# Kernel optimization log

Measured on AMD Instinct MI355X. Metric: run time of the kernel, lower is better.

## Reference

```python
import jax, jax.numpy as jnp
import numpy as np

T, B, H, L = 256, 64, 1024, 2

def setup_inputs() -> dict:
    key = jax.random.key(0)
    ks = jax.random.split(key, 7)
    s = 1.0 / np.sqrt(H)  # torch LSTMCell init scale (uniform); randn*s keeps magnitudes sane
    return {
        "input_seq": jax.random.normal(ks[0], (T, B, H), jnp.float32),
        "h0": jax.random.normal(ks[1], (L, B, H), jnp.float32),
        "c0": jax.random.normal(ks[2], (L, B, H), jnp.float32),
        "W_ih": jax.random.normal(ks[3], (L, 4 * H, H), jnp.float32) * s,
        "W_hh": jax.random.normal(ks[4], (L, 4 * H, H), jnp.float32) * s,
        "b_ih": jax.random.normal(ks[5], (L, 4 * H), jnp.float32) * s,
        "b_hh": jax.random.normal(ks[6], (L, 4 * H), jnp.float32) * s,
    }

def _lstm_cell(x, h, c, w_ih, w_hh, bi, bh):
    # torch.nn.LSTMCell gate order: i, f, g, o
    gates = x @ w_ih.T + bi + h @ w_hh.T + bh  # [B, 4H]
    i, f, g, o = jnp.split(gates, 4, axis=-1)
    c_new = jax.nn.sigmoid(f) * c + jax.nn.sigmoid(i) * jnp.tanh(g)
    h_new = jax.nn.sigmoid(o) * jnp.tanh(c_new)
    return h_new, c_new

def reference(input_seq, h0, c0, W_ih, W_hh, b_ih, b_hh):
    def step(carry, x_t):
        h, c = carry  # each [L, B, H]
        new_h, new_c = [], []
        x = x_t
        for l in range(L):  # small fixed layer loop
            hl, cl = _lstm_cell(x, h[l], c[l], W_ih[l], W_hh[l], b_ih[l], b_hh[l])
            new_h.append(hl)
            new_c.append(cl)
            x = hl
        return (jnp.stack(new_h), jnp.stack(new_c)), None
    (h_fin, c_fin), _ = jax.lax.scan(step, (h0, c0), input_seq)
    return h_fin[-1]  # top-layer hidden at final timestep, [B, H]
```

## Files before the change

### kernel.cpp

```cpp
#include <hip/hip_runtime.h>

#define T_LEN 256
#define B_SZ  64
#define H_SZ  1024
#define G4H   4096
#define HB    (B_SZ * H_SZ)
#define NBLK  256
#define RING_SLOTS (T_LEN + 1)

typedef __attribute__((ext_vector_type(8))) short short8;
typedef __attribute__((ext_vector_type(4))) float float4_;
typedef __attribute__((ext_vector_type(4))) unsigned int uint4_;

__device__ __forceinline__ unsigned short bf16_rne(float x) {
  unsigned u = __builtin_bit_cast(unsigned, x);
  unsigned r = u + 0x7FFFu + ((u >> 16) & 1u);
  return (unsigned short)(r >> 16);
}
__device__ __forceinline__ float bf16_to_f32(unsigned short s) {
  unsigned u = ((unsigned)s) << 16;
  return __builtin_bit_cast(float, u);
}

__global__ __launch_bounds__(256)
void init_h(const float* __restrict__ h0, unsigned short* __restrict__ ringb,
            unsigned* __restrict__ bar) {
  if (blockIdx.x == 0) {
    #pragma unroll
    for (int j = 0; j < 4; ++j) bar[threadIdx.x * 4 + j] = 0u;
  }
  const int e0 = (blockIdx.x * 256 + threadIdx.x) * 4;
  #pragma unroll
  for (int j = 0; j < 4; ++j) {
    const int e = e0 + j;
    const int l = e >> 16;
    const int rem = e & (HB - 1);
    ringb[((size_t)l * RING_SLOTS + T_LEN) * HB + rem] = bf16_rne(h0[e]);
  }
}

__device__ __forceinline__ void wave_poll_chunk(const unsigned* slots16,
                                               unsigned v, int lane) {
  for (;;) {
    unsigned s = 0xFFFFFFFFu;
    if (lane < 16)
      s = __hip_atomic_load(slots16 + lane, __ATOMIC_RELAXED,
                            __HIP_MEMORY_SCOPE_AGENT);
    if (__all((int)(s >= v))) return;
    __builtin_amdgcn_s_sleep(1);
  }
}

__device__ __forceinline__ void mfma3(float4_ (&acc)[4][2],
                                      const short8& hi, const short8& lo,
                                      const short8 (&wp)[2][2][4],
                                      const int m, const int kb) {
  #pragma unroll
  for (int nt = 0; nt < 2; ++nt) {
    acc[m][nt] = __builtin_amdgcn_mfma_f32_16x16x32_bf16(hi, wp[0][nt][kb], acc[m][nt], 0, 0, 0);
    acc[m][nt] = __builtin_amdgcn_mfma_f32_16x16x32_bf16(lo, wp[0][nt][kb], acc[m][nt], 0, 0, 0);
    acc[m][nt] = __builtin_amdgcn_mfma_f32_16x16x32_bf16(hi, wp[1][nt][kb], acc[m][nt], 0, 0, 0);
  }
}

__device__ __forceinline__ void accum_hb(float4_ (&acc)[4][2],
                                         const unsigned short* src,
                                         const short8 (&wp)[2][2][4],
                                         const int nn, const int quad,
                                         const int wave) {
  const int kbase = wave * 128 + quad * 8;
  short8 va[8], vb[8];
  #pragma unroll
  for (int kb = 0; kb < 2; ++kb)
    #pragma unroll
    for (int m = 0; m < 4; ++m)
      va[kb * 4 + m] = *(const short8*)(src + (size_t)(m * 16 + nn) * H_SZ +
                                        kbase + kb * 32);
  #pragma unroll
  for (int kb = 0; kb < 2; ++kb)
    #pragma unroll
    for (int m = 0; m < 4; ++m)
      vb[kb * 4 + m] = *(const short8*)(src + (size_t)(m * 16 + nn) * H_SZ +
                                        kbase + (kb + 2) * 32);
  #pragma unroll
  for (int kb = 0; kb < 2; ++kb)
    #pragma unroll
    for (int m = 0; m < 4; ++m)
      #pragma unroll
      for (int nt = 0; nt < 2; ++nt) {
        acc[m][nt] = __builtin_amdgcn_mfma_f32_16x16x32_bf16(va[kb * 4 + m], wp[0][nt][kb], acc[m][nt], 0, 0, 0);
        acc[m][nt] = __builtin_amdgcn_mfma_f32_16x16x32_bf16(va[kb * 4 + m], wp[1][nt][kb], acc[m][nt], 0, 0, 0);
      }
  #pragma unroll
  for (int kb = 0; kb < 2; ++kb)
    #pragma unroll
    for (int m = 0; m < 4; ++m)
      #pragma unroll
      for (int nt = 0; nt < 2; ++nt) {
        acc[m][nt] = __builtin_amdgcn_mfma_f32_16x16x32_bf16(vb[kb * 4 + m], wp[0][nt][kb + 2], acc[m][nt], 0, 0, 0);
        acc[m][nt] = __builtin_amdgcn_mfma_f32_16x16x32_bf16(vb[kb * 4 + m], wp[1][nt][kb + 2], acc[m][nt], 0, 0, 0);
      }
}

__device__ __forceinline__ void accum_x(float4_ (&acc)[4][2],
                                        const float* src,
                                        const short8 (&wp)[2][2][4],
                                        const int nn, const int quad,
                                        const int wave) {
  #pragma unroll
  for (int kb = 0; kb < 4; ++kb) {
    const int k0 = wave * 128 + kb * 32 + quad * 8;
    #pragma unroll
    for (int m = 0; m < 4; ++m) {
      const float* p = src + (size_t)(m * 16 + nn) * H_SZ + k0;
      short8 hi, lo;
      #pragma unroll
      for (int j = 0; j < 8; ++j) {
        const float v = p[j];
        const unsigned short h = bf16_rne(v);
        hi[j] = (short)h;
        lo[j] = (short)bf16_rne(v - bf16_to_f32(h));
      }
      mfma3(acc, hi, lo, wp, m, kb);
    }
  }
}

__global__ __launch_bounds__(512, 1)
void lstm_persist(const float* __restrict__ x_in,
                  const float* __restrict__ c0_in,
                  const float* __restrict__ Wih,
                  const float* __restrict__ Whh,
                  const float* __restrict__ bih,
                  const float* __restrict__ bhh,
                  unsigned short* __restrict__ ringb,
                  float* __restrict__ out,
                  unsigned* __restrict__ bar)
{
  const int wg   = blockIdx.x;
  const int tid  = threadIdx.x;
  const int lane = tid & 63;
  const int wave = tid >> 6;

  const int layer = wg >> 7;
  const int cb    = wg & 127;
  const int nn    = lane & 15;
  const int quad  = lane >> 4;

  __shared__ float lds[8][64][36];

  int growA[2];
  #pragma unroll
  for (int nt = 0; nt < 2; ++nt) {
    const int q = nt * 2 + (nn >> 3);
    growA[nt] = q * H_SZ + cb * 8 + (nn & 7);
  }

  short8 wreg[2][2][2][4];
  #pragma unroll
  for (int mat = 0; mat < 2; ++mat) {
    const float* wsrc = mat ? Whh : Wih;
    #pragma unroll
    for (int nt = 0; nt < 2; ++nt)
      #pragma unroll
      for (int kb = 0; kb < 4; ++kb) {
        const float* p = wsrc + ((size_t)layer * G4H + growA[nt]) * H_SZ +
                         wave * 128 + kb * 32 + quad * 8;
        short8 hi, lo;
        #pragma unroll
        for (int j = 0; j < 8; ++j) {
          const float v = p[j];
          const unsigned short h = bf16_rne(v);
          hi[j] = (short)h;
          lo[j] = (short)bf16_rne(v - bf16_to_f32(h));
        }
        wreg[mat][0][nt][kb] = hi;
        wreg[mat][1][nt][kb] = lo;
      }
  }

  const int eb   = tid >> 2;
  const int ec   = (tid & 3) * 2;
  const int ecol = cb * 8 + ec;
  float4_ biasA, biasB;
  #pragma unroll
  for (int q = 0; q < 4; ++q) {
    biasA[q] = bih[layer * G4H + q * H_SZ + ecol] +
               bhh[layer * G4H + q * H_SZ + ecol];
    biasB[q] = bih[layer * G4H + q * H_SZ + ecol + 1] +
               bhh[layer * G4H + q * H_SZ + ecol + 1];
  }

  unsigned*       slotp     = bar + layer * 128 + cb;
  const unsigned* chunk_own = bar + layer * 128 + wave * 16;
  const unsigned* chunk_l0  = bar + wave * 16;

  const unsigned short* ring_own = ringb + (size_t)layer * RING_SLOTS * HB;
  const unsigned short* ring_l0  = ringb;

  float cA = 0.f, cB = 0.f;
  float4_ acc[4][2];
  #pragma unroll
  for (int m = 0; m < 4; ++m)
    #pragma unroll
    for (int nt = 0; nt < 2; ++nt)
      acc[m][nt] = float4_{0.f, 0.f, 0.f, 0.f};

  if (layer == 0) {
    accum_x(acc, x_in, wreg[0], nn, quad, wave);
  } else {
    wave_poll_chunk(chunk_l0, 1u, lane);
    accum_hb(acc, ring_l0 , wreg[0], nn, quad, wave);
  }

  #pragma unroll 1
  for (int t = 0; t < T_LEN; ++t) {
    if (t > 0)
      wave_poll_chunk(chunk_own, (unsigned)t, lane);

    accum_hb(acc, ring_own + (size_t)(t ? t - 1 : T_LEN) * HB,
             wreg[1], nn, quad, wave);

    #pragma unroll
    for (int m = 0; m < 4; ++m)
      #pragma unroll
      for (int nt = 0; nt < 2; ++nt)
        #pragma unroll
        for (int r = 0; r < 4; ++r)
          lds[wave][m * 16 + quad * 4 + r]
             [((nn & 7) << 2) + nt * 2 + (nn >> 3)] = acc[m][nt][r];
    __syncthreads();

    if (tid < 256) {
      float4_ gA = biasA, gB = biasB;
      #pragma unroll
      for (int w = 0; w < 8; ++w) {
        gA += *(const float4_*)&lds[w][eb][ec * 4];
        gB += *(const float4_*)&lds[w][eb][ec * 4 + 4];
      }
      float cpA, cpB;
      if (t == 0) {
        cpA = c0_in[(size_t)layer * HB + (size_t)eb * H_SZ + ecol];
        cpB = c0_in[(size_t)layer * HB + (size_t)eb * H_SZ + ecol + 1];
      } else { cpA = cA; cpB = cB; }
      const float igA = 1.f / (1.f + __expf(-gA[0]));
      const float fgA = 1.f / (1.f + __expf(-gA[1]));
      const float ggA = tanhf(gA[2]);
      const float ogA = 1.f / (1.f + __expf(-gA[3]));
      const float cnA = fgA * cpA + igA * ggA;
      const float hnA = ogA * tanhf(cnA);
      const float igB = 1.f / (1.f + __expf(-gB[0]));
      const float fgB = 1.f / (1.f + __expf(-gB[1]));
      const float ggB = tanhf(gB[2]);
      const float ogB = 1.f / (1.f + __expf(-gB[3]));
      const float cnB = fgB * cpB + igB * ggB;
      const float hnB = ogB * tanhf(cnB);
      cA = cnA; cB = cnB;
      const size_t ridx = ((size_t)layer * RING_SLOTS + t) * HB +
                          (size_t)eb * H_SZ + ecol;
      const unsigned pk = (unsigned)bf16_rne(hnA) |
                          ((unsigned)bf16_rne(hnB) << 16);
      __hip_atomic_store((unsigned*)(ringb + ridx), pk,
                         __ATOMIC_RELAXED, __HIP_MEMORY_SCOPE_AGENT);
      if (layer == 1 && t == T_LEN - 1) {
        out[(size_t)eb * H_SZ + ecol]     = hnA;
        out[(size_t)eb * H_SZ + ecol + 1] = hnB;
      }
    }

    __syncthreads();
    if (tid == 0) {
      __builtin_amdgcn_s_waitcnt(0);
      __hip_atomic_store(slotp, (unsigned)(t + 1),
                         __ATOMIC_RELAXED, __HIP_MEMORY_SCOPE_AGENT);
    }

    if (t < T_LEN - 1) {
      #pragma unroll
      for (int m = 0; m < 4; ++m)
        #pragma unroll
        for (int nt = 0; nt < 2; ++nt)
          acc[m][nt] = float4_{0.f, 0.f, 0.f, 0.f};
      if (layer == 0) {
        accum_x(acc, x_in + (size_t)(t + 1) * HB, wreg[0], nn, quad, wave);
      } else {
        wave_poll_chunk(chunk_l0, (unsigned)(t + 2), lane);
        accum_hb(acc, ring_l0 + (size_t)(t + 1) * HB,
                 wreg[0], nn, quad, wave);
      }
    }
  }
}

extern "C" void kernel_launch(void* const* d_in, const int* in_sizes, int n_in,
                              void* d_out, int out_size, void* d_ws, size_t ws_size,
                              hipStream_t stream) {
  (void)in_sizes; (void)n_in; (void)out_size; (void)ws_size;
  const float* x   = (const float*)d_in[0];
  const float* h0  = (const float*)d_in[1];
  const float* c0  = (const float*)d_in[2];
  const float* Wih = (const float*)d_in[3];
  const float* Whh = (const float*)d_in[4];
  const float* bih = (const float*)d_in[5];
  const float* bhh = (const float*)d_in[6];
  float* out = (float*)d_out;

  char* w = (char*)d_ws;
  unsigned short* ringb = (unsigned short*)w;
  unsigned*       bar   = (unsigned*)(w + (size_t)2 * RING_SLOTS * HB * 2);

  init_h<<<2 * HB / 4 / 256, 256, 0, stream>>>(h0, ringb, bar);
  lstm_persist<<<NBLK, 512, 0, stream>>>(x, c0, Wih, Whh, bih, bhh,
                                         ringb, out, bar);
}
```

Baseline: 4.284 ms.

## Use per-wave completion flags, double-buffer LDS, and pre-pack x into bf16 hi/lo

Each block previously published one step flag after a second __syncthreads. Now each of the four elementwise waves publishes its own sub-flag once its stores drain, and consumers poll 64 flags per wave. The gate LDS buffer is double-buffered by timestep parity so the trailing block barrier can be dropped. Separately, a new pre-kernel splits x into packed bf16 hi/lo pairs, so the recurrent loop only does a wide load and byte permutes instead of per-element conversion. The cost is an extra full pass over x, a larger workspace, and wider polling traffic.

After: 3.675 ms. 14.2% less time.

```diff
diff --git a/kernel.cpp b/kernel.cpp
--- a/kernel.cpp
+++ b/kernel.cpp
@@ -11,6 +11,7 @@
 typedef __attribute__((ext_vector_type(8))) short short8;
 typedef __attribute__((ext_vector_type(4))) float float4_;
 typedef __attribute__((ext_vector_type(4))) unsigned int uint4_;
+typedef __attribute__((ext_vector_type(8))) unsigned int uint8_;
 
 __device__ __forceinline__ unsigned short bf16_rne(float x) {
   unsigned u = __builtin_bit_cast(unsigned, x);
@@ -20,6 +21,20 @@
 __device__ __forceinline__ float bf16_to_f32(unsigned short s) {
   unsigned u = ((unsigned)s) << 16;
   return __builtin_bit_cast(float, u);
+}
+
+__global__ __launch_bounds__(256)
+void pack_x(const float* __restrict__ src, unsigned* __restrict__ dst) {
+  const size_t i = ((size_t)blockIdx.x * 256 + threadIdx.x) * 4;
+  float4_ v = *(const float4_*)(src + i);
+  uint4_ o;
+  #pragma unroll
+  for (int j = 0; j < 4; ++j) {
+    const unsigned short h = bf16_rne(v[j]);
+    const unsigned short l = bf16_rne(v[j] - bf16_to_f32(h));
+    o[j] = (unsigned)h | ((unsigned)l << 16);
+  }
+  *(uint4_*)(dst + i) = o;
 }
 
 __global__ __launch_bounds__(256)
@@ -39,27 +54,13 @@
   }
 }
 
-__device__ __forceinline__ void wave_poll_chunk(const unsigned* slots16,
-                                               unsigned v, int lane) {
+__device__ __forceinline__ void wave_poll64(const unsigned* s64, unsigned v,
+                                            int lane) {
   for (;;) {
-    unsigned s = 0xFFFFFFFFu;
-    if (lane < 16)
-      s = __hip_atomic_load(slots16 + lane, __ATOMIC_RELAXED,
-                            __HIP_MEMORY_SCOPE_AGENT);
+    const unsigned s = __hip_atomic_load(s64 + lane, __ATOMIC_RELAXED,
+                                         __HIP_MEMORY_SCOPE_AGENT);
     if (__all((int)(s >= v))) return;
     __builtin_amdgcn_s_sleep(1);
-  }
-}
-
-__device__ __forceinline__ void mfma3(float4_ (&acc)[4][2],
-                                      const short8& hi, const short8& lo,
-                                      const short8 (&wp)[2][2][4],
-                                      const int m, const int kb) {
-  #pragma unroll
-  for (int nt = 0; nt < 2; ++nt) {
-    acc[m][nt] = __builtin_amdgcn_mfma_f32_16x16x32_bf16(hi, wp[0][nt][kb], acc[m][nt], 0, 0, 0);
-    acc[m][nt] = __builtin_amdgcn_mfma_f32_16x16x32_bf16(lo, wp[0][nt][kb], acc[m][nt], 0, 0, 0);
-    acc[m][nt] = __builtin_amdgcn_mfma_f32_16x16x32_bf16(hi, wp[1][nt][kb], acc[m][nt], 0, 0, 0);
   }
 }
 
@@ -69,65 +70,55 @@
                                          const int nn, const int quad,
                                          const int wave) {
   const int kbase = wave * 128 + quad * 8;
-  short8 va[8], vb[8];
-  #pragma unroll
-  for (int kb = 0; kb < 2; ++kb)
+  short8 v[16];
+  #pragma unroll
+  for (int kb = 0; kb < 4; ++kb)
     #pragma unroll
     for (int m = 0; m < 4; ++m)
-      va[kb * 4 + m] = *(const short8*)(src + (size_t)(m * 16 + nn) * H_SZ +
-                                        kbase + kb * 32);
-  #pragma unroll
-  for (int kb = 0; kb < 2; ++kb)
+      v[kb * 4 + m] = *(const short8*)(src + (size_t)(m * 16 + nn) * H_SZ +
+                                       kbase + kb * 32);
+  #pragma unroll
+  for (int kb = 0; kb < 4; ++kb)
     #pragma unroll
     for (int m = 0; m < 4; ++m)
-      vb[kb * 4 + m] = *(const short8*)(src + (size_t)(m * 16 + nn) * H_SZ +
-                                        kbase + (kb + 2) * 32);
-  #pragma unroll
-  for (int kb = 0; kb < 2; ++kb)
-    #pragma unroll
-    for (int m = 0; m < 4; ++m)
       #pragma unroll
       for (int nt = 0; nt < 2; ++nt) {
-        acc[m][nt] = __builtin_amdgcn_mfma_f32_16x16x32_bf16(va[kb * 4 + m], wp[0][nt][kb], acc[m][nt], 0, 0, 0);
-        acc[m][nt] = __builtin_amdgcn_mfma_f32_16x16x32_bf16(va[kb * 4 + m], wp[1][nt][kb], acc[m][nt], 0, 0, 0);
-      }
-  #pragma unroll
-  for (int kb = 0; kb < 2; ++kb)
-    #pragma unroll
-    for (int m = 0; m < 4; ++m)
-      #pragma unroll
-      for (int nt = 0; nt < 2; ++nt) {
-        acc[m][nt] = __builtin_amdgcn_mfma_f32_16x16x32_bf16(vb[kb * 4 + m], wp[0][nt][kb + 2], acc[m][nt], 0, 0, 0);
-        acc[m][nt] = __builtin_amdgcn_mfma_f32_16x16x32_bf16(vb[kb * 4 + m], wp[1][nt][kb + 2], acc[m][nt], 0, 0, 0);
-      }
-}
-
-__device__ __forceinline__ void accum_x(float4_ (&acc)[4][2],
-                                        const float* src,
-                                        const short8 (&wp)[2][2][4],
-                                        const int nn, const int quad,
-                                        const int wave) {
+        acc[m][nt] = __builtin_amdgcn_mfma_f32_16x16x32_bf16(v[kb * 4 + m], wp[0][nt][kb], acc[m][nt], 0, 0, 0);
+        acc[m][nt] = __builtin_amdgcn_mfma_f32_16x16x32_bf16(v[kb * 4 + m], wp[1][nt][kb], acc[m][nt], 0, 0, 0);
+      }
+}
+
+__device__ __forceinline__ void accum_xp(float4_ (&acc)[4][2],
+                                         const unsigned* src,
+                                         const short8 (&wp)[2][2][4],
+                                         const int nn, const int quad,
+                                         const int wave) {
   #pragma unroll
   for (int kb = 0; kb < 4; ++kb) {
     const int k0 = wave * 128 + kb * 32 + quad * 8;
     #pragma unroll
     for (int m = 0; m < 4; ++m) {
-      const float* p = src + (size_t)(m * 16 + nn) * H_SZ + k0;
-      short8 hi, lo;
-      #pragma unroll
-      for (int j = 0; j < 8; ++j) {
-        const float v = p[j];
-        const unsigned short h = bf16_rne(v);
-        hi[j] = (short)h;
-        lo[j] = (short)bf16_rne(v - bf16_to_f32(h));
-      }
-      mfma3(acc, hi, lo, wp, m, kb);
+      const uint8_ u = *(const uint8_*)(src + (size_t)(m * 16 + nn) * H_SZ + k0);
+      uint4_ h4, l4;
+      #pragma unroll
+      for (int r = 0; r < 4; ++r) {
+        h4[r] = __builtin_amdgcn_perm(u[2 * r + 1], u[2 * r], 0x05040100u);
+        l4[r] = __builtin_amdgcn_perm(u[2 * r + 1], u[2 * r], 0x07060302u);
+      }
+      const short8 hi = __builtin_bit_cast(short8, h4);
+      const short8 lo = __builtin_bit_cast(short8, l4);
+      #pragma unroll
+      for (int nt = 0; nt < 2; ++nt) {
+        acc[m][nt] = __builtin_amdgcn_mfma_f32_16x16x32_bf16(hi, wp[0][nt][kb], acc[m][nt], 0, 0, 0);
+        acc[m][nt] = __builtin_amdgcn_mfma_f32_16x16x32_bf16(lo, wp[0][nt][kb], acc[m][nt], 0, 0, 0);
+        acc[m][nt] = __builtin_amdgcn_mfma_f32_16x16x32_bf16(hi, wp[1][nt][kb], acc[m][nt], 0, 0, 0);
+      }
     }
   }
 }
 
 __global__ __launch_bounds__(512, 1)
-void lstm_persist(const float* __restrict__ x_in,
+void lstm_persist(const unsigned* __restrict__ xp,
                   const float* __restrict__ c0_in,
                   const float* __restrict__ Wih,
                   const float* __restrict__ Whh,
@@ -147,7 +138,7 @@
   const int nn    = lane & 15;
   const int quad  = lane >> 4;
 
-  __shared__ float lds[8][64][36];
+  __shared__ float lds[2][8][64][36];
 
   int growA[2];
   #pragma unroll
@@ -179,8 +170,8 @@
       }
   }
 
-  const int eb   = tid >> 2;
-  const int ec   = (tid & 3) * 2;
+  const int eb   = wave * 16 + (lane >> 2);
+  const int ec   = (lane & 3) * 2;
   const int ecol = cb * 8 + ec;
   float4_ biasA, biasB;
   #pragma unroll
@@ -191,9 +182,9 @@
                bhh[layer * G4H + q * H_SZ + ecol + 1];
   }
 
-  unsigned*       slotp     = bar + layer * 128 + cb;
-  const unsigned* chunk_own = bar + layer * 128 + wave * 16;
-  const unsigned* chunk_l0  = bar + wave * 16;
+  unsigned*       subflag   = bar + layer * 512 + cb * 4 + wave;
+  const unsigned* chunk_own = bar + layer * 512 + wave * 64;
+  const unsigned* chunk_l0  = bar + wave * 64;
 
   const unsigned short* ring_own = ringb + (size_t)layer * RING_SLOTS * HB;
   const unsigned short* ring_l0  = ringb;
@@ -207,36 +198,37 @@
       acc[m][nt] = float4_{0.f, 0.f, 0.f, 0.f};
 
   if (layer == 0) {
-    accum_x(acc, x_in, wreg[0], nn, quad, wave);
+    accum_xp(acc, xp, wreg[0], nn, quad, wave);
   } else {
-    wave_poll_chunk(chunk_l0, 1u, lane);
+    wave_poll64(chunk_l0, 1u, lane);
     accum_hb(acc, ring_l0 , wreg[0], nn, quad, wave);
   }
 
   #pragma unroll 1
   for (int t = 0; t < T_LEN; ++t) {
     if (t > 0)
-      wave_poll_chunk(chunk_own, (unsigned)t, lane);
+      wave_poll64(chunk_own, (unsigned)t, lane);
 
     accum_hb(acc, ring_own + (size_t)(t ? t - 1 : T_LEN) * HB,
              wreg[1], nn, quad, wave);
 
+    float (*ldsb)[64][36] = lds[t & 1];
     #pragma unroll
     for (int m = 0; m < 4; ++m)
       #pragma unroll
       for (int nt = 0; nt < 2; ++nt)
         #pragma unroll
         for (int r = 0; r < 4; ++r)
-          lds[wave][m * 16 + quad * 4 + r]
-             [((nn & 7) << 2) + nt * 2 + (nn >> 3)] = acc[m][nt][r];
+          ldsb[wave][m * 16 + quad * 4 + r]
+              [((nn & 7) << 2) + nt * 2 + (nn >> 3)] = acc[m][nt][r];
     __syncthreads();
 
-    if (tid < 256) {
+    if (wave < 4) {
       float4_ gA = biasA, gB = biasB;
       #pragma unroll
       for (int w = 0; w < 8; ++w) {
-        gA += *(const float4_*)&lds[w][eb][ec * 4];
-        gB += *(const float4_*)&lds[w][eb][ec * 4 + 4];
+        gA += *(const float4_*)&ldsb[w][eb][ec * 4];
+        gB += *(const float4_*)&ldsb[w][eb][ec * 4 + 4];
       }
       float cpA, cpB;
       if (t == 0) {
@@ -266,13 +258,10 @@
         out[(size_t)eb * H_SZ + ecol]     = hnA;
         out[(size_t)eb * H_SZ + ecol + 1] = hnB;
       }
-    }
-
-    __syncthreads();
-    if (tid == 0) {
-      __builtin_amdgcn_s_waitcnt(0);
-      __hip_atomic_store(slotp, (unsigned)(t + 1),
-                         __ATOMIC_RELAXED, __HIP_MEMORY_SCOPE_AGENT);
+      asm volatile("s_waitcnt vmcnt(0)" ::: "memory");
+      if (lane == 0)
+        __hip_atomic_store(subflag, (unsigned)(t + 1),
+                           __ATOMIC_RELAXED, __HIP_MEMORY_SCOPE_AGENT);
     }
 
     if (t < T_LEN - 1) {
@@ -282,9 +271,9 @@
         for (int nt = 0; nt < 2; ++nt)
           acc[m][nt] = float4_{0.f, 0.f, 0.f, 0.f};
       if (layer == 0) {
-        accum_x(acc, x_in + (size_t)(t + 1) * HB, wreg[0], nn, quad, wave);
+        accum_xp(acc, xp + (size_t)(t + 1) * HB, wreg[0], nn, quad, wave);
       } else {
-        wave_poll_chunk(chunk_l0, (unsigned)(t + 2), lane);
+        wave_poll64(chunk_l0, (unsigned)(t + 2), lane);
         accum_hb(acc, ring_l0 + (size_t)(t + 1) * HB,
                  wreg[0], nn, quad, wave);
       }
@@ -306,10 +295,13 @@
   float* out = (float*)d_out;
 
   char* w = (char*)d_ws;
-  unsigned short* ringb = (unsigned short*)w;
-  unsigned*       bar   = (unsigned*)(w + (size_t)2 * RING_SLOTS * HB * 2);
-
+  unsigned*       xpack = (unsigned*)w;
+  unsigned short* ringb = (unsigned short*)(w + (size_t)T_LEN * HB * 4);
+  unsigned*       bar   = (unsigned*)(w + (size_t)T_LEN * HB * 4
+                                        + (size_t)2 * RING_SLOTS * HB * 2);
+
+  pack_x<<<(T_LEN * HB) / 4 / 256, 256, 0, stream>>>(x, xpack);
   init_h<<<2 * HB / 4 / 256, 256, 0, stream>>>(h0, ringb, bar);
-  lstm_persist<<<NBLK, 512, 0, stream>>>(x, c0, Wih, Whh, bih, bhh,
+  lstm_persist<<<NBLK, 512, 0, stream>>>(xpack, c0, Wih, Whh, bih, bhh,
                                          ringb, out, bar);
 }
```
